# Kernel tuning notes

Measured on AMD Instinct MI355X. Metric: run time of the kernel, lower is better.

## Reference

```python
import jax, jax.numpy as jnp
import numpy as np

# anchor encoding indices: [x,y,z,log w,log l,log h,sin,cos,vx,vy,vz]
NUM_HEADS = 8
LN_EPS = 1e-5


def layer_norm(x, g, b):
    mu = jnp.mean(x, axis=-1, keepdims=True)
    var = jnp.var(x, axis=-1, keepdims=True)
    return (x - mu) * jax.lax.rsqrt(var + LN_EPS) * g + b


def align_anchors_to_frame(anchor, Tm):
    # anchor: (..., N, 11), Tm: (..., 4, 4)
    R = Tm[..., :3, :3]
    t = Tm[..., :3, 3]
    center = jnp.einsum('...ij,...nj->...ni', R, anchor[..., 0:3]) + t[..., None, :]
    size = anchor[..., 3:6]
    yaw = jnp.einsum('...ij,...nj->...ni', R[..., :2, :2], anchor[..., 6:8])
    vel = jnp.einsum('...ij,...nj->...ni', R, anchor[..., 8:11])
    return jnp.concatenate([center, size, yaw, vel], axis=-1)


def setup_inputs() -> dict:
    key = jax.random.key(0)
    ks = jax.random.split(key, 12)
    B, T, N, C, E, A = 2, 12, 1024, 256, 256, 11
    inp = {
        'seq_features': jax.random.normal(ks[0], (B, T, N, C), jnp.float32),
        'seq_anchors': jax.random.normal(ks[1], (B, T, N, A), jnp.float32),
        'T_ego_his2cur': jax.random.normal(ks[2], (B, T, 4, 4), jnp.float32),
        'Wf': jax.random.normal(ks[3], (E, C), jnp.float32) * (C ** -0.5),
        'bf': jnp.zeros((E,), jnp.float32),
        'Wa': jax.random.normal(ks[4], (E, A), jnp.float32) * (A ** -0.5),
        'ba': jnp.zeros((E,), jnp.float32),
        'Win': jax.random.normal(ks[5], (3 * E, E), jnp.float32) * (E ** -0.5),
        'bin_': jnp.zeros((3 * E,), jnp.float32),
        'gamma': jnp.ones((E,), jnp.float32),
        'beta': jnp.zeros((E,), jnp.float32),
    }
    return inp


def reference(seq_features, seq_anchors, T_ego_his2cur, Wf, bf, Wa, ba, Win, bin_, gamma, beta):
    B, T, N, C = seq_features.shape
    E = gamma.shape[0]
    H = NUM_HEADS
    D = E // H

    feat_cur = seq_features[:, 1:]    # (B,T-1,N,C)
    feat_prev = seq_features[:, :-1]
    anc_cur = seq_anchors[:, 1:]
    anc_prev = align_anchors_to_frame(seq_anchors[:, :-1], T_ego_his2cur[:, 1:])

    tok_cur = layer_norm(feat_cur @ Wf.T + bf + anc_cur @ Wa.T + ba, gamma, beta)
    tok_prev = layer_norm(feat_prev @ Wf.T + bf + anc_prev @ Wa.T + ba, gamma, beta)

    Wq, Wk = Win[:E], Win[E:2 * E]
    bq, bk = bin_[:E], bin_[E:2 * E]
    scale = np.float32(D) ** np.float32(-0.5)
    q = ((tok_cur @ Wq.T + bq) * scale).reshape(B, T - 1, N, H, D)
    k = (tok_prev @ Wk.T + bk).reshape(B, T - 1, N, H, D)

    scores = jnp.einsum('btnhd,btmhd->bthnm', q, k)  # (B,T-1,H,N,N)
    attn = jax.nn.softmax(scores, axis=-1).mean(axis=2)  # head-averaged weights

    eye = jnp.broadcast_to(jnp.eye(N, dtype=seq_features.dtype), (B, 1, N, N))
    return jnp.concatenate([eye, attn], axis=1)  # (B,T,N,N)
```

## Files before the change

### kernel.cpp

```cpp
#include <hip/hip_runtime.h>
#include <hip/hip_bf16.h>
#include <math.h>

#define LN_EPS 1e-5f

typedef short bf16x8 __attribute__((ext_vector_type(8)));
typedef float f32x4 __attribute__((ext_vector_type(4)));

__device__ inline short f2bf(float f) {
  union { float f; unsigned u; } v; v.f = f;
  unsigned r = v.u + 0x7FFFu + ((v.u >> 16) & 1u);
  return (short)(r >> 16);
}
__device__ inline float bf2f(unsigned short s) {
  union { unsigned u; float f; } v; v.u = ((unsigned)s) << 16;
  return v.f;
}
__device__ inline float fast_exp2(float x) {
#if __has_builtin(__builtin_amdgcn_exp2f)
  return __builtin_amdgcn_exp2f(x);
#else
  return __expf(x * 0.69314718056f);
#endif
}

__global__ __launch_bounds__(256) void convert_kernel(const float* __restrict__ sf,
    const float* __restrict__ Wf, const float* __restrict__ Win,
    short* __restrict__ sfb, short* __restrict__ Wfb, short* __restrict__ Wqkb)
{
  size_t i = ((size_t)blockIdx.x * 256 + threadIdx.x) * 8;
  const float* src;
  short* dst;
  if (i < 6291456) { src = sf + i; dst = sfb + i; }
  else if (i < 6356992) { src = Wf + (i - 6291456); dst = Wfb + (i - 6291456); }
  else { src = Win + (i - 6356992); dst = Wqkb + (i - 6356992); }
  f32x4 x0 = *(const f32x4*)src;
  f32x4 x1 = *(const f32x4*)(src + 4);
  bf16x8 v;
  v[0] = f2bf(x0[0]); v[1] = f2bf(x0[1]); v[2] = f2bf(x0[2]); v[3] = f2bf(x0[3]);
  v[4] = f2bf(x1[0]); v[5] = f2bf(x1[1]); v[6] = f2bf(x1[2]); v[7] = f2bf(x1[3]);
  *(bf16x8*)dst = v;
}

__global__ __launch_bounds__(256) void gemm_feat(const short* __restrict__ Ap,
    const short* __restrict__ W, const float* __restrict__ bias,
    short* __restrict__ Out)
{
  __shared__ short lda[128][40];
  __shared__ short ldb[128][40];
  const int tid = threadIdx.x;
  const int bm = blockIdx.x * 128, bn = blockIdx.y * 128;
  const int wid = tid >> 6, lane = tid & 63;
  const int quad = lane >> 4, l15 = lane & 15;
  const int wm = (wid & 1) * 64, wn = (wid >> 1) * 64;
  const int srow = tid >> 2, sseg = tid & 3;

  f32x4 z = {0.f, 0.f, 0.f, 0.f};
  f32x4 acc[4][4];
  #pragma unroll
  for (int i = 0; i < 4; ++i)
    #pragma unroll
    for (int j = 0; j < 4; ++j) acc[i][j] = z;

  const short* a0 = Ap + (size_t)(bm + srow) * 256 + sseg * 8;
  const short* a1 = Ap + (size_t)(bm + srow + 64) * 256 + sseg * 8;
  const short* b0 = W + (size_t)(bn + srow) * 256 + sseg * 8;
  const short* b1 = W + (size_t)(bn + srow + 64) * 256 + sseg * 8;

  for (int kk = 0; kk < 256; kk += 32) {
    *(bf16x8*)&lda[srow][sseg * 8]      = *(const bf16x8*)(a0 + kk);
    *(bf16x8*)&lda[srow + 64][sseg * 8] = *(const bf16x8*)(a1 + kk);
    *(bf16x8*)&ldb[srow][sseg * 8]      = *(const bf16x8*)(b0 + kk);
    *(bf16x8*)&ldb[srow + 64][sseg * 8] = *(const bf16x8*)(b1 + kk);
    __syncthreads();
    bf16x8 af[4], bq[4];
    #pragma unroll
    for (int i = 0; i < 4; ++i) {
      af[i] = *(const bf16x8*)&lda[wm + i * 16 + l15][quad * 8];
      bq[i] = *(const bf16x8*)&ldb[wn + i * 16 + l15][quad * 8];
    }
    #pragma unroll
    for (int i = 0; i < 4; ++i)
      #pragma unroll
      for (int j = 0; j < 4; ++j)
        acc[i][j] = __builtin_amdgcn_mfma_f32_16x16x32_bf16(af[i], bq[j], acc[i][j], 0, 0, 0);
    __syncthreads();
  }

  #pragma unroll
  for (int i = 0; i < 4; ++i)
    #pragma unroll
    for (int j = 0; j < 4; ++j)
      #pragma unroll
      for (int r = 0; r < 4; ++r) {
        int grow = bm + wm + i * 16 + quad * 4 + r;
        int gcol = bn + wn + j * 16 + l15;
        Out[(size_t)grow * 256 + gcol] = f2bf(acc[i][j][r] + bias[gcol]);
      }
}

__global__ __launch_bounds__(256) void gemm_qk(const short* __restrict__ tokc,
    const short* __restrict__ tokp, const short* __restrict__ Wqkb,
    const float* __restrict__ binv, short* __restrict__ qb, short* __restrict__ kb)
{
  const int sel = blockIdx.z;
  const short* Ap = sel ? tokp : tokc;
  const short* W = Wqkb + (size_t)sel * 65536;
  const float* bias = binv + sel * 256;
  const float alpha = sel ? 1.0f : 0.17677669529663687f * 1.4426950408889634f;
  short* Out = sel ? kb : qb;

  __shared__ short lda[128][40];
  __shared__ short ldb[128][40];
  const int tid = threadIdx.x;
  const int bm = blockIdx.x * 128, bn = blockIdx.y * 128;
  const int wid = tid >> 6, lane = tid & 63;
  const int quad = lane >> 4, l15 = lane & 15;
  const int wm = (wid & 1) * 64, wn = (wid >> 1) * 64;
  const int srow = tid >> 2, sseg = tid & 3;

  f32x4 z = {0.f, 0.f, 0.f, 0.f};
  f32x4 acc[4][4];
  #pragma unroll
  for (int i = 0; i < 4; ++i)
    #pragma unroll
    for (int j = 0; j < 4; ++j) acc[i][j] = z;

  const short* a0 = Ap + (size_t)(bm + srow) * 256 + sseg * 8;
  const short* a1 = Ap + (size_t)(bm + srow + 64) * 256 + sseg * 8;
  const short* b0 = W + (size_t)(bn + srow) * 256 + sseg * 8;
  const short* b1 = W + (size_t)(bn + srow + 64) * 256 + sseg * 8;

  for (int kk = 0; kk < 256; kk += 32) {
    *(bf16x8*)&lda[srow][sseg * 8]      = *(const bf16x8*)(a0 + kk);
    *(bf16x8*)&lda[srow + 64][sseg * 8] = *(const bf16x8*)(a1 + kk);
    *(bf16x8*)&ldb[srow][sseg * 8]      = *(const bf16x8*)(b0 + kk);
    *(bf16x8*)&ldb[srow + 64][sseg * 8] = *(const bf16x8*)(b1 + kk);
    __syncthreads();
    bf16x8 af[4], bq[4];
    #pragma unroll
    for (int i = 0; i < 4; ++i) {
      af[i] = *(const bf16x8*)&lda[wm + i * 16 + l15][quad * 8];
      bq[i] = *(const bf16x8*)&ldb[wn + i * 16 + l15][quad * 8];
    }
    #pragma unroll
    for (int i = 0; i < 4; ++i)
      #pragma unroll
      for (int j = 0; j < 4; ++j)
        acc[i][j] = __builtin_amdgcn_mfma_f32_16x16x32_bf16(af[i], bq[j], acc[i][j], 0, 0, 0);
    __syncthreads();
  }

  #pragma unroll
  for (int i = 0; i < 4; ++i)
    #pragma unroll
    for (int j = 0; j < 4; ++j)
      #pragma unroll
      for (int r = 0; r < 4; ++r) {
        int grow = bm + wm + i * 16 + quad * 4 + r;
        int gcol = bn + wn + j * 16 + l15;
        float v = (acc[i][j][r] + bias[gcol]) * alpha;
        int btr = grow >> 10, nn = grow & 1023, h = gcol >> 5, d = gcol & 31;
        Out[(((size_t)btr * 8 + h) * 1024 + nn) * 32 + d] = f2bf(v);
      }
}

__global__ __launch_bounds__(256) void anchor_ln(const short* __restrict__ featproj,
  const float* __restrict__ anchors, const float* __restrict__ Tego,
  const float* __restrict__ Wa, const float* __restrict__ ba,
  const float* __restrict__ gamma, const float* __restrict__ beta,
  short* __restrict__ tok_cur, short* __restrict__ tok_prev)
{
  const int wid = threadIdx.x >> 6, lane = threadIdx.x & 63;
  const int tok = blockIdx.x * 4 + wid;
  const int which = tok >= 22528 ? 1 : 0;
  const int rem = tok - which * 22528;
  const int bt = rem >> 10;
  const int n = rem & 1023;
  const int b = bt / 11, t = bt - b * 11;
  const int tt = which ? t : t + 1;

  const float* ap = anchors + (((size_t)b * 12 + tt) * 1024 + n) * 11;
  float a[11];
  #pragma unroll
  for (int j = 0; j < 11; ++j) a[j] = ap[j];
  if (which) {
    const float* Tm = Tego + ((size_t)b * 12 + t + 1) * 16;
    float r00 = Tm[0], r01 = Tm[1], r02 = Tm[2],  t0 = Tm[3];
    float r10 = Tm[4], r11 = Tm[5], r12 = Tm[6],  t1 = Tm[7];
    float r20 = Tm[8], r21 = Tm[9], r22 = Tm[10], t2 = Tm[11];
    float a0 = a[0], a1 = a[1], a2 = a[2];
    float a6 = a[6], a7 = a[7], a8 = a[8], a9 = a[9], a10 = a[10];
    a[0] = r00 * a0 + r01 * a1 + r02 * a2 + t0;
    a[1] = r10 * a0 + r11 * a1 + r12 * a2 + t1;
    a[2] = r20 * a0 + r21 * a1 + r22 * a2 + t2;
    a[6] = r00 * a6 + r01 * a7;
    a[7] = r10 * a6 + r11 * a7;
    a[8] = r00 * a8 + r01 * a9 + r02 * a10;
    a[9] = r10 * a8 + r11 * a9 + r12 * a10;
    a[10] = r20 * a8 + r21 * a9 + r22 * a10;
  }

  const int c0 = lane * 4;
  const size_t frow = (((size_t)b * 12 + tt) * 1024 + n) * 256 + c0;
  ushort4 raw = *(const ushort4*)(featproj + frow);
  f32x4 bav = *(const f32x4*)(ba + c0);
  float v[4];
  v[0] = bf2f(raw.x) + bav[0]; v[1] = bf2f(raw.y) + bav[1];
  v[2] = bf2f(raw.z) + bav[2]; v[3] = bf2f(raw.w) + bav[3];
  #pragma unroll
  for (int c = 0; c < 4; ++c) {
    const float* war = Wa + (size_t)(c0 + c) * 11;
    float acc = 0.f;
    #pragma unroll
    for (int j = 0; j < 11; ++j) acc += war[j] * a[j];
    v[c] += acc;
  }
  float s1 = v[0] + v[1] + v[2] + v[3];
  float s2 = v[0]*v[0] + v[1]*v[1] + v[2]*v[2] + v[3]*v[3];
  #pragma unroll
  for (int off = 1; off < 64; off <<= 1) { s1 += __shfl_xor(s1, off); s2 += __shfl_xor(s2, off); }
  float mean = s1 * (1.0f / 256.0f);
  float var = s2 * (1.0f / 256.0f) - mean * mean;
  float rstd = rsqrtf(var + LN_EPS);
  f32x4 gv = *(const f32x4*)(gamma + c0);
  f32x4 bv = *(const f32x4*)(beta + c0);
  ushort4 o;
  o.x = (unsigned short)f2bf((v[0] - mean) * rstd * gv[0] + bv[0]);
  o.y = (unsigned short)f2bf((v[1] - mean) * rstd * gv[1] + bv[1]);
  o.z = (unsigned short)f2bf((v[2] - mean) * rstd * gv[2] + bv[2]);
  o.w = (unsigned short)f2bf((v[3] - mean) * rstd * gv[3] + bv[3]);
  short* dst = which ? tok_prev : tok_cur;
  *(ushort4*)(dst + ((size_t)bt * 1024 + n) * 256 + c0) = o;
}

__global__ __launch_bounds__(256) void denom_kernel(const short* __restrict__ q,
  const short* __restrict__ k, float* __restrict__ dinv)
{
  __shared__ short kst[2][4096];
  const int tid = threadIdx.x, wid = tid >> 6, lane = tid & 63;
  const int quad = lane >> 4, l15 = lane & 15;
  const int h = blockIdx.y, bt = blockIdx.z;
  const int n0 = blockIdx.x * 128 + wid * 32;
  const size_t base = ((size_t)bt * 8 + h) * 1024 * 32;
  bf16x8 qf0 = *(const bf16x8*)(q + base + (size_t)(n0 + l15) * 32 + quad * 8);
  bf16x8 qf1 = *(const bf16x8*)(q + base + (size_t)(n0 + 16 + l15) * 32 + quad * 8);
  const short* ksA = k + base + (size_t)(wid * 16) * 32 + lane * 8;
  const short* ksB = k + base + (size_t)((wid + 4) * 16) * 32 + lane * 8;
  const int wswz = ((lane & 3) ^ ((lane >> 3) & 3)) * 8;
  const int rswz = (quad ^ ((l15 >> 1) & 3)) * 8;
  short* lwA = &kst[0][wid * 512 + (lane >> 2) * 32 + wswz];
  short* lwB = &kst[0][(wid + 4) * 512 + (lane >> 2) * 32 + wswz];

  f32x4 z = {0.f, 0.f, 0.f, 0.f};
  float sum0[4] = {0.f, 0.f, 0.f, 0.f};
  float sum1[4] = {0.f, 0.f, 0.f, 0.f};

  bf16x8 stA = *(const bf16x8*)ksA;
  bf16x8 stB = *(const bf16x8*)ksB;
  *(bf16x8*)lwA = stA;
  *(bf16x8*)lwB = stB;
  __syncthreads();

  #pragma unroll 1
  for (int rd = 0; rd < 8; ++rd) {
    const int buf = rd & 1;
    if (rd < 7) {
      stA = *(const bf16x8*)(ksA + (size_t)(rd + 1) * 128 * 32);
      stB = *(const bf16x8*)(ksB + (size_t)(rd + 1) * 128 * 32);
    }
    #pragma unroll
    for (int s = 0; s < 8; ++s) {
      bf16x8 kf = *(const bf16x8*)&kst[buf][s * 512 + l15 * 32 + rswz];
      f32x4 sc0 = __builtin_amdgcn_mfma_f32_16x16x32_bf16(qf0, kf, z, 0, 0, 0);
      f32x4 sc1 = __builtin_amdgcn_mfma_f32_16x16x32_bf16(qf1, kf, z, 0, 0, 0);
      #pragma unroll
      for (int r = 0; r < 4; ++r) {
        sum0[r] += fast_exp2(sc0[r]);
        sum1[r] += fast_exp2(sc1[r]);
      }
    }
    if (rd < 7) {
      *(bf16x8*)(lwA + ((buf ^ 1) << 12)) = stA;
      *(bf16x8*)(lwB + ((buf ^ 1) << 12)) = stB;
    }
    __syncthreads();
  }
  #pragma unroll
  for (int off = 1; off < 16; off <<= 1) {
    #pragma unroll
    for (int r = 0; r < 4; ++r) {
      sum0[r] += __shfl_xor(sum0[r], off);
      sum1[r] += __shfl_xor(sum1[r], off);
    }
  }
  if (l15 == 0) {
    float* dp = dinv + ((size_t)bt * 8 + h) * 1024 + n0 + quad * 4;
    #pragma unroll
    for (int r = 0; r < 4; ++r) {
      dp[r] = 1.f / sum0[r];
      dp[16 + r] = 1.f / sum1[r];
    }
  }
}

__global__ __launch_bounds__(256) void prob_kernel(const short* __restrict__ q,
  const short* __restrict__ k, const float* __restrict__ dinv, float* __restrict__ out)
{
  __shared__ short kst[2][4096];
  const int tid = threadIdx.x, wid = tid >> 6, lane = tid & 63;
  const int quad = lane >> 4, l15 = lane & 15;
  const int bt = blockIdx.z;
  const int n0 = blockIdx.x * 64 + wid * 16;
  const int mbase = blockIdx.y * 128;
  const int b = bt / 11, t = bt - b * 11;
  bf16x8 qf[8];
  float invd[8][4];
  #pragma unroll
  for (int h = 0; h < 8; ++h) {
    const size_t base = ((size_t)bt * 8 + h) * 1024 * 32;
    qf[h] = *(const bf16x8*)(q + base + (size_t)(n0 + l15) * 32 + quad * 8);
    const float* dp = dinv + ((size_t)bt * 8 + h) * 1024 + n0 + quad * 4;
    #pragma unroll
    for (int r = 0; r < 4; ++r) invd[h][r] = dp[r] * 0.125f;
  }
  const short* ksA = k + (((size_t)bt * 8 + wid    ) * 1024 + mbase) * 32 + lane * 8;
  const short* ksB = k + (((size_t)bt * 8 + wid + 4) * 1024 + mbase) * 32 + lane * 8;
  const int wswz = ((lane & 3) ^ ((lane >> 3) & 3)) * 8;
  const int rswz = (quad ^ ((l15 >> 1) & 3)) * 8;
  short* lwA = &kst[0][wid * 512 + (lane >> 2) * 32 + wswz];
  short* lwB = &kst[0][(wid + 4) * 512 + (lane >> 2) * 32 + wswz];

  float* ob = out + ((size_t)(b * 12 + t + 1)) * 1024 * 1024
                  + (size_t)(n0 + quad * 4) * 1024 + l15;
  f32x4 z = {0.f, 0.f, 0.f, 0.f};

  bf16x8 stA = *(const bf16x8*)ksA;
  bf16x8 stB = *(const bf16x8*)ksB;
  *(bf16x8*)lwA = stA;
  *(bf16x8*)lwB = stB;
  __syncthreads();

  #pragma unroll 1
  for (int mt = 0; mt < 8; ++mt) {
    const int buf = mt & 1;
    if (mt < 7) {
      stA = *(const bf16x8*)(ksA + (size_t)(mt + 1) * 16 * 32);
      stB = *(const bf16x8*)(ksB + (size_t)(mt + 1) * 16 * 32);
    }
    float P0 = 0, P1 = 0, P2 = 0, P3 = 0;
    #pragma unroll
    for (int h = 0; h < 8; ++h) {
      bf16x8 kf = *(const bf16x8*)&kst[buf][h * 512 + l15 * 32 + rswz];
      f32x4 s = __builtin_amdgcn_mfma_f32_16x16x32_bf16(qf[h], kf, z, 0, 0, 0);
      P0 += fast_exp2(s[0]) * invd[h][0];
      P1 += fast_exp2(s[1]) * invd[h][1];
      P2 += fast_exp2(s[2]) * invd[h][2];
      P3 += fast_exp2(s[3]) * invd[h][3];
    }
    float* op = ob + mbase + mt * 16;
    op[0] = P0; op[1024] = P1; op[2048] = P2; op[3072] = P3;
    if (mt < 7) {
      *(bf16x8*)(lwA + ((buf ^ 1) << 12)) = stA;
      *(bf16x8*)(lwB + ((buf ^ 1) << 12)) = stB;
    }
    __syncthreads();
  }
}

__global__ __launch_bounds__(256) void eye_kernel(float* __restrict__ out) {
  int gid = blockIdx.x * 256 + threadIdx.x;
  int b = gid >> 18, rem = gid & 262143;
  int n = rem >> 8, m4 = rem & 255;
  f32x4 v = {0.f, 0.f, 0.f, 0.f};
  int c = n - m4 * 4;
  if (c >= 0 && c < 4) v[c] = 1.0f;
  *(f32x4*)(out + (size_t)b * 12582912 + (size_t)n * 1024 + m4 * 4) = v;
}

extern "C" void kernel_launch(void* const* d_in, const int* in_sizes, int n_in,
                              void* d_out, int out_size, void* d_ws, size_t ws_size,
                              hipStream_t stream)
{
  const float* sf   = (const float*)d_in[0];
  const float* sa   = (const float*)d_in[1];
  const float* te   = (const float*)d_in[2];
  const float* Wf   = (const float*)d_in[3];
  const float* bfv  = (const float*)d_in[4];
  const float* Wa   = (const float*)d_in[5];
  const float* ba   = (const float*)d_in[6];
  const float* Win  = (const float*)d_in[7];
  const float* binv = (const float*)d_in[8];
  const float* gam  = (const float*)d_in[9];
  const float* bet  = (const float*)d_in[10];
  float* out = (float*)d_out;

  char* w = (char*)d_ws;
  short* featproj = (short*)w;  w += 12582912;
  short* tok_cur  = (short*)w;  w += 11534336;
  short* tok_prev = (short*)w;  w += 11534336;
  short* qb       = (short*)w;  w += 11534336;
  short* kb       = (short*)w;  w += 11534336;
  float* dinv     = (float*)w;  w += 720896;
  short* sfb      = (short*)w;  w += 12582912;
  short* Wfb      = (short*)w;  w += 131072;
  short* Wqkb     = (short*)w;  w += 262144;

  convert_kernel<<<dim3(3168), 256, 0, stream>>>(sf, Wf, Win, sfb, Wfb, Wqkb);
  gemm_feat<<<dim3(192, 2), 256, 0, stream>>>(sfb, Wfb, bfv, featproj);
  anchor_ln<<<dim3(11264), 256, 0, stream>>>(featproj, sa, te, Wa, ba, gam, bet, tok_cur, tok_prev);
  gemm_qk<<<dim3(176, 2, 2), 256, 0, stream>>>(tok_cur, tok_prev, Wqkb, binv, qb, kb);
  denom_kernel<<<dim3(8, 8, 22), 256, 0, stream>>>(qb, kb, dinv);
  prob_kernel<<<dim3(16, 8, 22), 256, 0, stream>>>(qb, kb, dinv, out);
  eye_kernel<<<dim3(2048), 256, 0, stream>>>(out);
}
```

Baseline: 263.5 us.

## Fuse feature GEMM with anchor projection and LayerNorm, transpose score MFMAs for vector stores

Replaces the separate fp32-to-bf16 conversion of features, the feature GEMM and the anchor/LayerNorm kernel with one kernel. It converts features on the fly, computes a full 256-wide row tile, adds the anchor projection and applies LayerNorm, and writes each frame once as the current token and once as the previous token. This removes the featproj and sfb intermediates and two launches. The denominator and probability kernels now swap the MFMA operands so that each lane holds four consecutive key columns, which allows 16-byte output stores and cheaper reductions; the probability kernel handles 32 query rows per wave. The fused kernel launches only 384 blocks and recomputes the anchor dot products twice, which may limit occupancy.

```diff
diff --git a/kernel.cpp b/kernel.cpp
--- a/kernel.cpp
+++ b/kernel.cpp
@@ -24,16 +24,14 @@
 #endif
 }
 
-__global__ __launch_bounds__(256) void convert_kernel(const float* __restrict__ sf,
-    const float* __restrict__ Wf, const float* __restrict__ Win,
-    short* __restrict__ sfb, short* __restrict__ Wfb, short* __restrict__ Wqkb)
+__global__ __launch_bounds__(256) void convert_kernel(const float* __restrict__ Wf,
+    const float* __restrict__ Win, short* __restrict__ Wfb, short* __restrict__ Wqkb)
 {
   size_t i = ((size_t)blockIdx.x * 256 + threadIdx.x) * 8;
   const float* src;
   short* dst;
-  if (i < 6291456) { src = sf + i; dst = sfb + i; }
-  else if (i < 6356992) { src = Wf + (i - 6291456); dst = Wfb + (i - 6291456); }
-  else { src = Win + (i - 6356992); dst = Wqkb + (i - 6356992); }
+  if (i < 65536) { src = Wf + i; dst = Wfb + i; }
+  else { src = Win + (i - 65536); dst = Wqkb + (i - 65536); }
   f32x4 x0 = *(const f32x4*)src;
   f32x4 x1 = *(const f32x4*)(src + 4);
   bf16x8 v;
@@ -42,10 +40,162 @@
   *(bf16x8*)dst = v;
 }
 
-__global__ __launch_bounds__(256) void gemm_feat(const short* __restrict__ Ap,
-    const short* __restrict__ W, const float* __restrict__ bias,
-    short* __restrict__ Out)
-{
+__global__ __launch_bounds__(256) void feat_ln(const float* __restrict__ Af,
+    const short* __restrict__ Wb, const float* __restrict__ bfv,
+    const float* __restrict__ anchors, const float* __restrict__ Tego,
+    const float* __restrict__ Wa, const float* __restrict__ ba,
+    const float* __restrict__ gamma, const float* __restrict__ beta,
+    short* __restrict__ tok_cur, short* __restrict__ tok_prev)
+{
+  __shared__ short lda[64][40];
+  __shared__ short ldb[256][40];
+  __shared__ float aC[64][12];
+  __shared__ float aP[64][12];
+  const int tid = threadIdx.x;
+  const int wid = tid >> 6, lane = tid & 63;
+  const int quad = lane >> 4, l15 = lane & 15;
+  const int row0 = blockIdx.x * 64;
+  const int s24 = row0 >> 10;
+  const int b = s24 / 12, t = s24 - b * 12;
+  const int n0 = row0 & 1023;
+  const int srow = tid >> 2, sseg = tid & 3;
+
+  if (tid < 64) {
+    const float* ap = anchors + ((size_t)s24 * 1024 + n0 + tid) * 11;
+    float a[11];
+    #pragma unroll
+    for (int j = 0; j < 11; ++j) a[j] = ap[j];
+    #pragma unroll
+    for (int j = 0; j < 11; ++j) aC[tid][j] = a[j];
+    if (t <= 10) {
+      const float* Tm = Tego + ((size_t)b * 12 + t + 1) * 16;
+      float r00 = Tm[0], r01 = Tm[1], r02 = Tm[2],  t0 = Tm[3];
+      float r10 = Tm[4], r11 = Tm[5], r12 = Tm[6],  t1 = Tm[7];
+      float r20 = Tm[8], r21 = Tm[9], r22 = Tm[10], t2 = Tm[11];
+      aP[tid][0] = r00 * a[0] + r01 * a[1] + r02 * a[2] + t0;
+      aP[tid][1] = r10 * a[0] + r11 * a[1] + r12 * a[2] + t1;
+      aP[tid][2] = r20 * a[0] + r21 * a[1] + r22 * a[2] + t2;
+      aP[tid][3] = a[3]; aP[tid][4] = a[4]; aP[tid][5] = a[5];
+      aP[tid][6] = r00 * a[6] + r01 * a[7];
+      aP[tid][7] = r10 * a[6] + r11 * a[7];
+      aP[tid][8] = r00 * a[8] + r01 * a[9] + r02 * a[10];
+      aP[tid][9] = r10 * a[8] + r11 * a[9] + r12 * a[10];
+      aP[tid][10] = r20 * a[8] + r21 * a[9] + r22 * a[10];
+    }
+  }
+
+  f32x4 z = {0.f, 0.f, 0.f, 0.f};
+  f32x4 acc[16];
+  #pragma unroll
+  for (int j = 0; j < 16; ++j) acc[j] = z;
+
+  const float* ap0 = Af + (size_t)(row0 + srow) * 256 + sseg * 8;
+  const short* wp = Wb + (size_t)srow * 256 + sseg * 8;
+
+  for (int kk = 0; kk < 256; kk += 32) {
+    {
+      f32x4 x0 = *(const f32x4*)(ap0 + kk);
+      f32x4 x1 = *(const f32x4*)(ap0 + kk + 4);
+      bf16x8 vv;
+      vv[0] = f2bf(x0[0]); vv[1] = f2bf(x0[1]); vv[2] = f2bf(x0[2]); vv[3] = f2bf(x0[3]);
+      vv[4] = f2bf(x1[0]); vv[5] = f2bf(x1[1]); vv[6] = f2bf(x1[2]); vv[7] = f2bf(x1[3]);
+      *(bf16x8*)&lda[srow][sseg * 8] = vv;
+    }
+    #pragma unroll
+    for (int p = 0; p < 4; ++p)
+      *(bf16x8*)&ldb[srow + 64 * p][sseg * 8] =
+          *(const bf16x8*)(wp + (size_t)p * 64 * 256 + kk);
+    __syncthreads();
+    bf16x8 af = *(const bf16x8*)&lda[wid * 16 + l15][quad * 8];
+    #pragma unroll
+    for (int j = 0; j < 16; ++j) {
+      bf16x8 bq = *(const bf16x8*)&ldb[j * 16 + l15][quad * 8];
+      acc[j] = __builtin_amdgcn_mfma_f32_16x16x32_bf16(af, bq, acc[j], 0, 0, 0);
+    }
+    __syncthreads();
+  }
+
+  float cb[16];
+  #pragma unroll
+  for (int j = 0; j < 16; ++j) {
+    int col = j * 16 + l15;
+    cb[j] = bfv[col] + ba[col];
+  }
+
+  auto emit = [&](const float (*aS)[12], short* dst, size_t tokbase) {
+    float arow[4][11];
+    #pragma unroll
+    for (int r = 0; r < 4; ++r)
+      #pragma unroll
+      for (int jj = 0; jj < 11; ++jj)
+        arow[r][jj] = aS[wid * 16 + quad * 4 + r][jj];
+    float s1[4] = {0.f, 0.f, 0.f, 0.f};
+    float s2[4] = {0.f, 0.f, 0.f, 0.f};
+    #pragma unroll
+    for (int j = 0; j < 16; ++j) {
+      const float* war = Wa + (size_t)(j * 16 + l15) * 11;
+      float wa[11];
+      #pragma unroll
+      for (int jj = 0; jj < 11; ++jj) wa[jj] = war[jj];
+      #pragma unroll
+      for (int r = 0; r < 4; ++r) {
+        float d = 0.f;
+        #pragma unroll
+        for (int jj = 0; jj < 11; ++jj) d += wa[jj] * arow[r][jj];
+        float v = acc[j][r] + cb[j] + d;
+        s1[r] += v; s2[r] += v * v;
+      }
+    }
+    #pragma unroll
+    for (int r = 0; r < 4; ++r) {
+      #pragma unroll
+      for (int off = 1; off < 16; off <<= 1) {
+        s1[r] += __shfl_xor(s1[r], off);
+        s2[r] += __shfl_xor(s2[r], off);
+      }
+    }
+    float mean[4], rstd[4];
+    #pragma unroll
+    for (int r = 0; r < 4; ++r) {
+      mean[r] = s1[r] * (1.0f / 256.0f);
+      float var = s2[r] * (1.0f / 256.0f) - mean[r] * mean[r];
+      rstd[r] = rsqrtf(var + LN_EPS);
+    }
+    #pragma unroll
+    for (int j = 0; j < 16; ++j) {
+      int col = j * 16 + l15;
+      const float* war = Wa + (size_t)col * 11;
+      float wa[11];
+      #pragma unroll
+      for (int jj = 0; jj < 11; ++jj) wa[jj] = war[jj];
+      float g = gamma[col], be = beta[col];
+      #pragma unroll
+      for (int r = 0; r < 4; ++r) {
+        float d = 0.f;
+        #pragma unroll
+        for (int jj = 0; jj < 11; ++jj) d += wa[jj] * arow[r][jj];
+        float v = acc[j][r] + cb[j] + d;
+        int n = n0 + wid * 16 + quad * 4 + r;
+        dst[(tokbase + n) * 256 + col] = f2bf((v - mean[r]) * rstd[r] * g + be);
+      }
+    }
+  };
+
+  if (t >= 1)  emit(aC, tok_cur,  (size_t)(b * 11 + t - 1) * 1024);
+  if (t <= 10) emit(aP, tok_prev, (size_t)(b * 11 + t) * 1024);
+}
+
+__global__ __launch_bounds__(256) void gemm_qk(const short* __restrict__ tokc,
+    const short* __restrict__ tokp, const short* __restrict__ Wqkb,
+    const float* __restrict__ binv, short* __restrict__ qb, short* __restrict__ kb)
+{
+  const int sel = blockIdx.z;
+  const short* Ap = sel ? tokp : tokc;
+  const short* W = Wqkb + (size_t)sel * 65536;
+  const float* bias = binv + sel * 256;
+  const float alpha = sel ? 1.0f : 0.17677669529663687f * 1.4426950408889634f;
+  short* Out = sel ? kb : qb;
+
   __shared__ short lda[128][40];
   __shared__ short ldb[128][40];
   const int tid = threadIdx.x;
@@ -95,143 +245,10 @@
       for (int r = 0; r < 4; ++r) {
         int grow = bm + wm + i * 16 + quad * 4 + r;
         int gcol = bn + wn + j * 16 + l15;
-        Out[(size_t)grow * 256 + gcol] = f2bf(acc[i][j][r] + bias[gcol]);
-      }
-}
-
-__global__ __launch_bounds__(256) void gemm_qk(const short* __restrict__ tokc,
-    const short* __restrict__ tokp, const short* __restrict__ Wqkb,
-    const float* __restrict__ binv, short* __restrict__ qb, short* __restrict__ kb)
-{
-  const int sel = blockIdx.z;
-  const short* Ap = sel ? tokp : tokc;
-  const short* W = Wqkb + (size_t)sel * 65536;
-  const float* bias = binv + sel * 256;
-  const float alpha = sel ? 1.0f : 0.17677669529663687f * 1.4426950408889634f;
-  short* Out = sel ? kb : qb;
-
-  __shared__ short lda[128][40];
-  __shared__ short ldb[128][40];
-  const int tid = threadIdx.x;
-  const int bm = blockIdx.x * 128, bn = blockIdx.y * 128;
-  const int wid = tid >> 6, lane = tid & 63;
-  const int quad = lane >> 4, l15 = lane & 15;
-  const int wm = (wid & 1) * 64, wn = (wid >> 1) * 64;
-  const int srow = tid >> 2, sseg = tid & 3;
-
-  f32x4 z = {0.f, 0.f, 0.f, 0.f};
-  f32x4 acc[4][4];
-  #pragma unroll
-  for (int i = 0; i < 4; ++i)
-    #pragma unroll
-    for (int j = 0; j < 4; ++j) acc[i][j] = z;
-
-  const short* a0 = Ap + (size_t)(bm + srow) * 256 + sseg * 8;
-  const short* a1 = Ap + (size_t)(bm + srow + 64) * 256 + sseg * 8;
-  const short* b0 = W + (size_t)(bn + srow) * 256 + sseg * 8;
-  const short* b1 = W + (size_t)(bn + srow + 64) * 256 + sseg * 8;
-
-  for (int kk = 0; kk < 256; kk += 32) {
-    *(bf16x8*)&lda[srow][sseg * 8]      = *(const bf16x8*)(a0 + kk);
-    *(bf16x8*)&lda[srow + 64][sseg * 8] = *(const bf16x8*)(a1 + kk);
-    *(bf16x8*)&ldb[srow][sseg * 8]      = *(const bf16x8*)(b0 + kk);
-    *(bf16x8*)&ldb[srow + 64][sseg * 8] = *(const bf16x8*)(b1 + kk);
-    __syncthreads();
-    bf16x8 af[4], bq[4];
-    #pragma unroll
-    for (int i = 0; i < 4; ++i) {
-      af[i] = *(const bf16x8*)&lda[wm + i * 16 + l15][quad * 8];
-      bq[i] = *(const bf16x8*)&ldb[wn + i * 16 + l15][quad * 8];
-    }
-    #pragma unroll
-    for (int i = 0; i < 4; ++i)
-      #pragma unroll
-      for (int j = 0; j < 4; ++j)
-        acc[i][j] = __builtin_amdgcn_mfma_f32_16x16x32_bf16(af[i], bq[j], acc[i][j], 0, 0, 0);
-    __syncthreads();
-  }
-
-  #pragma unroll
-  for (int i = 0; i < 4; ++i)
-    #pragma unroll
-    for (int j = 0; j < 4; ++j)
-      #pragma unroll
-      for (int r = 0; r < 4; ++r) {
-        int grow = bm + wm + i * 16 + quad * 4 + r;
-        int gcol = bn + wn + j * 16 + l15;
         float v = (acc[i][j][r] + bias[gcol]) * alpha;
         int btr = grow >> 10, nn = grow & 1023, h = gcol >> 5, d = gcol & 31;
         Out[(((size_t)btr * 8 + h) * 1024 + nn) * 32 + d] = f2bf(v);
       }
-}
-
-__global__ __launch_bounds__(256) void anchor_ln(const short* __restrict__ featproj,
-  const float* __restrict__ anchors, const float* __restrict__ Tego,
-  const float* __restrict__ Wa, const float* __restrict__ ba,
-  const float* __restrict__ gamma, const float* __restrict__ beta,
-  short* __restrict__ tok_cur, short* __restrict__ tok_prev)
-{
-  const int wid = threadIdx.x >> 6, lane = threadIdx.x & 63;
-  const int tok = blockIdx.x * 4 + wid;
-  const int which = tok >= 22528 ? 1 : 0;
-  const int rem = tok - which * 22528;
-  const int bt = rem >> 10;
-  const int n = rem & 1023;
-  const int b = bt / 11, t = bt - b * 11;
-  const int tt = which ? t : t + 1;
-
-  const float* ap = anchors + (((size_t)b * 12 + tt) * 1024 + n) * 11;
-  float a[11];
-  #pragma unroll
-  for (int j = 0; j < 11; ++j) a[j] = ap[j];
-  if (which) {
-    const float* Tm = Tego + ((size_t)b * 12 + t + 1) * 16;
-    float r00 = Tm[0], r01 = Tm[1], r02 = Tm[2],  t0 = Tm[3];
-    float r10 = Tm[4], r11 = Tm[5], r12 = Tm[6],  t1 = Tm[7];
-    float r20 = Tm[8], r21 = Tm[9], r22 = Tm[10], t2 = Tm[11];
-    float a0 = a[0], a1 = a[1], a2 = a[2];
-    float a6 = a[6], a7 = a[7], a8 = a[8], a9 = a[9], a10 = a[10];
-    a[0] = r00 * a0 + r01 * a1 + r02 * a2 + t0;
-    a[1] = r10 * a0 + r11 * a1 + r12 * a2 + t1;
-    a[2] = r20 * a0 + r21 * a1 + r22 * a2 + t2;
-    a[6] = r00 * a6 + r01 * a7;
-    a[7] = r10 * a6 + r11 * a7;
-    a[8] = r00 * a8 + r01 * a9 + r02 * a10;
-    a[9] = r10 * a8 + r11 * a9 + r12 * a10;
-    a[10] = r20 * a8 + r21 * a9 + r22 * a10;
-  }
-
-  const int c0 = lane * 4;
-  const size_t frow = (((size_t)b * 12 + tt) * 1024 + n) * 256 + c0;
-  ushort4 raw = *(const ushort4*)(featproj + frow);
-  f32x4 bav = *(const f32x4*)(ba + c0);
-  float v[4];
-  v[0] = bf2f(raw.x) + bav[0]; v[1] = bf2f(raw.y) + bav[1];
-  v[2] = bf2f(raw.z) + bav[2]; v[3] = bf2f(raw.w) + bav[3];
-  #pragma unroll
-  for (int c = 0; c < 4; ++c) {
-    const float* war = Wa + (size_t)(c0 + c) * 11;
-    float acc = 0.f;
-    #pragma unroll
-    for (int j = 0; j < 11; ++j) acc += war[j] * a[j];
-    v[c] += acc;
-  }
-  float s1 = v[0] + v[1] + v[2] + v[3];
-  float s2 = v[0]*v[0] + v[1]*v[1] + v[2]*v[2] + v[3]*v[3];
-  #pragma unroll
-  for (int off = 1; off < 64; off <<= 1) { s1 += __shfl_xor(s1, off); s2 += __shfl_xor(s2, off); }
-  float mean = s1 * (1.0f / 256.0f);
-  float var = s2 * (1.0f / 256.0f) - mean * mean;
-  float rstd = rsqrtf(var + LN_EPS);
-  f32x4 gv = *(const f32x4*)(gamma + c0);
-  f32x4 bv = *(const f32x4*)(beta + c0);
-  ushort4 o;
-  o.x = (unsigned short)f2bf((v[0] - mean) * rstd * gv[0] + bv[0]);
-  o.y = (unsigned short)f2bf((v[1] - mean) * rstd * gv[1] + bv[1]);
-  o.z = (unsigned short)f2bf((v[2] - mean) * rstd * gv[2] + bv[2]);
-  o.w = (unsigned short)f2bf((v[3] - mean) * rstd * gv[3] + bv[3]);
-  short* dst = which ? tok_prev : tok_cur;
-  *(ushort4*)(dst + ((size_t)bt * 1024 + n) * 256 + c0) = o;
 }
 
 __global__ __launch_bounds__(256) void denom_kernel(const short* __restrict__ q,
@@ -242,7 +259,7 @@
   const int quad = lane >> 4, l15 = lane & 15;
   const int h = blockIdx.y, bt = blockIdx.z;
   const int n0 = blockIdx.x * 128 + wid * 32;
-  const size_t base = ((size_t)bt * 8 + h) * 1024 * 32;
+  const size_t base = ((size_t)bt * 8 + h) * 32768;
   bf16x8 qf0 = *(const bf16x8*)(q + base + (size_t)(n0 + l15) * 32 + quad * 8);
   bf16x8 qf1 = *(const bf16x8*)(q + base + (size_t)(n0 + 16 + l15) * 32 + quad * 8);
   const short* ksA = k + base + (size_t)(wid * 16) * 32 + lane * 8;
@@ -253,8 +270,7 @@
   short* lwB = &kst[0][(wid + 4) * 512 + (lane >> 2) * 32 + wswz];
 
   f32x4 z = {0.f, 0.f, 0.f, 0.f};
-  float sum0[4] = {0.f, 0.f, 0.f, 0.f};
-  float sum1[4] = {0.f, 0.f, 0.f, 0.f};
+  float s0 = 0.f, s1 = 0.f;
 
   bf16x8 stA = *(const bf16x8*)ksA;
   bf16x8 stB = *(const bf16x8*)ksB;
@@ -272,13 +288,10 @@
     #pragma unroll
     for (int s = 0; s < 8; ++s) {
       bf16x8 kf = *(const bf16x8*)&kst[buf][s * 512 + l15 * 32 + rswz];
-      f32x4 sc0 = __builtin_amdgcn_mfma_f32_16x16x32_bf16(qf0, kf, z, 0, 0, 0);
-      f32x4 sc1 = __builtin_amdgcn_mfma_f32_16x16x32_bf16(qf1, kf, z, 0, 0, 0);
-      #pragma unroll
-      for (int r = 0; r < 4; ++r) {
-        sum0[r] += fast_exp2(sc0[r]);
-        sum1[r] += fast_exp2(sc1[r]);
-      }
+      f32x4 c0 = __builtin_amdgcn_mfma_f32_16x16x32_bf16(kf, qf0, z, 0, 0, 0);
+      f32x4 c1 = __builtin_amdgcn_mfma_f32_16x16x32_bf16(kf, qf1, z, 0, 0, 0);
+      s0 += fast_exp2(c0[0]) + fast_exp2(c0[1]) + fast_exp2(c0[2]) + fast_exp2(c0[3]);
+      s1 += fast_exp2(c1[0]) + fast_exp2(c1[1]) + fast_exp2(c1[2]) + fast_exp2(c1[3]);
     }
     if (rd < 7) {
       *(bf16x8*)(lwA + ((buf ^ 1) << 12)) = stA;
@@ -286,21 +299,12 @@
     }
     __syncthreads();
   }
-  #pragma unroll
-  for (int off = 1; off < 16; off <<= 1) {
-    #pragma unroll
-    for (int r = 0; r < 4; ++r) {
-      sum0[r] += __shfl_xor(sum0[r], off);
-      sum1[r] += __shfl_xor(sum1[r], off);
-    }
-  }
-  if (l15 == 0) {
-    float* dp = dinv + ((size_t)bt * 8 + h) * 1024 + n0 + quad * 4;
-    #pragma unroll
-    for (int r = 0; r < 4; ++r) {
-      dp[r] = 1.f / sum0[r];
-      dp[16 + r] = 1.f / sum1[r];
-    }
+  s0 += __shfl_xor(s0, 16); s0 += __shfl_xor(s0, 32);
+  s1 += __shfl_xor(s1, 16); s1 += __shfl_xor(s1, 32);
+  if (quad == 0) {
+    float* dp = dinv + ((size_t)bt * 8 + h) * 1024 + n0;
+    dp[l15] = 1.f / s0;
+    dp[16 + l15] = 1.f / s1;
   }
 }
 
@@ -311,18 +315,19 @@
   const int tid = threadIdx.x, wid = tid >> 6, lane = tid & 63;
   const int quad = lane >> 4, l15 = lane & 15;
   const int bt = blockIdx.z;
-  const int n0 = blockIdx.x * 64 + wid * 16;
+  const int n0 = blockIdx.x * 128 + wid * 32;
   const int mbase = blockIdx.y * 128;
   const int b = bt / 11, t = bt - b * 11;
-  bf16x8 qf[8];
-  float invd[8][4];
+
+  bf16x8 qf0[8], qf1[8];
+  float invd0[8], invd1[8];
   #pragma unroll
   for (int h = 0; h < 8; ++h) {
-    const size_t base = ((size_t)bt * 8 + h) * 1024 * 32;
-    qf[h] = *(const bf16x8*)(q + base + (size_t)(n0 + l15) * 32 + quad * 8);
-    const float* dp = dinv + ((size_t)bt * 8 + h) * 1024 + n0 + quad * 4;
-    #pragma unroll
-    for (int r = 0; r < 4; ++r) invd[h][r] = dp[r] * 0.125f;
+    const size_t base = ((size_t)bt * 8 + h) * 32768;
+    qf0[h] = *(const bf16x8*)(q + base + (size_t)(n0 + l15) * 32 + quad * 8);
+    qf1[h] = *(const bf16x8*)(q + base + (size_t)(n0 + 16 + l15) * 32 + quad * 8);
+    invd0[h] = dinv[((size_t)bt * 8 + h) * 1024 + n0 + l15] * 0.125f;
+    invd1[h] = dinv[((size_t)bt * 8 + h) * 1024 + n0 + 16 + l15] * 0.125f;
   }
   const short* ksA = k + (((size_t)bt * 8 + wid    ) * 1024 + mbase) * 32 + lane * 8;
   const short* ksB = k + (((size_t)bt * 8 + wid + 4) * 1024 + mbase) * 32 + lane * 8;
@@ -331,8 +336,9 @@
   short* lwA = &kst[0][wid * 512 + (lane >> 2) * 32 + wswz];
   short* lwB = &kst[0][(wid + 4) * 512 + (lane >> 2) * 32 + wswz];
 
-  float* ob = out + ((size_t)(b * 12 + t + 1)) * 1024 * 1024
-                  + (size_t)(n0 + quad * 4) * 1024 + l15;
+  float* ob0 = out + ((size_t)(b * 12 + t + 1) * 1024 + n0 + l15) * 1024
+                   + mbase + quad * 4;
+  float* ob1 = ob0 + (size_t)16 * 1024;
   f32x4 z = {0.f, 0.f, 0.f, 0.f};
 
   bf16x8 stA = *(const bf16x8*)ksA;
@@ -348,18 +354,20 @@
       stA = *(const bf16x8*)(ksA + (size_t)(mt + 1) * 16 * 32);
       stB = *(const bf16x8*)(ksB + (size_t)(mt + 1) * 16 * 32);
     }
-    float P0 = 0, P1 = 0, P2 = 0, P3 = 0;
+    f32x4 P0 = z, P1 = z;
     #pragma unroll
     for (int h = 0; h < 8; ++h) {
       bf16x8 kf = *(const bf16x8*)&kst[buf][h * 512 + l15 * 32 + rswz];
-      f32x4 s = __builtin_amdgcn_mfma_f32_16x16x32_bf16(qf[h], kf, z, 0, 0, 0);
-      P0 += fast_exp2(s[0]) * invd[h][0];
-      P1 += fast_exp2(s[1]) * invd[h][1];
-      P2 += fast_exp2(s[2]) * invd[h][2];
-      P3 += fast_exp2(s[3]) * invd[h][3];
-    }
-    float* op = ob + mbase + mt * 16;
-    op[0] = P0; op[1024] = P1; op[2048] = P2; op[3072] = P3;
+      f32x4 c0 = __builtin_amdgcn_mfma_f32_16x16x32_bf16(kf, qf0[h], z, 0, 0, 0);
+      f32x4 c1 = __builtin_amdgcn_mfma_f32_16x16x32_bf16(kf, qf1[h], z, 0, 0, 0);
+      #pragma unroll
+      for (int r = 0; r < 4; ++r) {
+        P0[r] += fast_exp2(c0[r]) * invd0[h];
+        P1[r] += fast_exp2(c1[r]) * invd1[h];
+      }
+    }
+    *(f32x4*)(ob0 + mt * 16) = P0;
+    *(f32x4*)(ob1 + mt * 16) = P1;
     if (mt < 7) {
       *(bf16x8*)(lwA + ((buf ^ 1) << 12)) = stA;
       *(bf16x8*)(lwB + ((buf ^ 1) << 12)) = stB;
@@ -396,21 +404,19 @@
   float* out = (float*)d_out;
 
   char* w = (char*)d_ws;
-  short* featproj = (short*)w;  w += 12582912;
   short* tok_cur  = (short*)w;  w += 11534336;
   short* tok_prev = (short*)w;  w += 11534336;
   short* qb       = (short*)w;  w += 11534336;
   short* kb       = (short*)w;  w += 11534336;
   float* dinv     = (float*)w;  w += 720896;
-  short* sfb      = (short*)w;  w += 12582912;
   short* Wfb      = (short*)w;  w += 131072;
   short* Wqkb     = (short*)w;  w += 262144;
 
-  convert_kernel<<<dim3(3168), 256, 0, stream>>>(sf, Wf, Win, sfb, Wfb, Wqkb);
-  gemm_feat<<<dim3(192, 2), 256, 0, stream>>>(sfb, Wfb, bfv, featproj);
-  anchor_ln<<<dim3(11264), 256, 0, stream>>>(featproj, sa, te, Wa, ba, gam, bet, tok_cur, tok_prev);
+  convert_kernel<<<dim3(96), 256, 0, stream>>>(Wf, Win, Wfb, Wqkb);
+  feat_ln<<<dim3(384), 256, 0, stream>>>(sf, Wfb, bfv, sa, te, Wa, ba, gam, bet,
+                                         tok_cur, tok_prev);
   gemm_qk<<<dim3(176, 2, 2), 256, 0, stream>>>(tok_cur, tok_prev, Wqkb, binv, qb, kb);
   denom_kernel<<<dim3(8, 8, 22), 256, 0, stream>>>(qb, kb, dinv);
-  prob_kernel<<<dim3(16, 8, 22), 256, 0, stream>>>(qb, kb, dinv, out);
+  prob_kernel<<<dim3(8, 8, 22), 256, 0, stream>>>(qb, kb, dinv, out);
   eye_kernel<<<dim3(2048), 256, 0, stream>>>(out);
 }
```

Result: no change. 261.7 us (-0.7%).
